# Kernel tuning notes

Hardware: AMD Instinct MI355X
Metric: run time of the kernel (lower is better)

## Reference

```python
import jax, jax.numpy as jnp
import numpy as np

EMBED = 1024
D_FF = 4 * EMBED
N_EXPERTS = 8
TOP_K = 2
B, S = 2, 1024


def setup_inputs() -> dict:
    key = jax.random.key(0)
    ks = jax.random.split(key, 10)
    sc_d = 1.0 / np.sqrt(EMBED)
    sc_h = 1.0 / np.sqrt(D_FF)
    return {
        "inputs": jax.random.normal(ks[0], (B, S, EMBED), jnp.float32),
        # router MLP: Linear(D,4D) -> ReLU -> Linear(4D,E)
        "rw1": jax.random.normal(ks[1], (EMBED, D_FF), jnp.float32) * sc_d,
        "rb1": jnp.zeros((D_FF,), jnp.float32),
        "rw2": jax.random.normal(ks[2], (D_FF, N_EXPERTS), jnp.float32) * sc_h,
        "rb2": jnp.zeros((N_EXPERTS,), jnp.float32),
        # stacked expert weights: Linear(D,4D) -> ReLU -> Linear(4D,D)
        "W1": jax.random.normal(ks[3], (N_EXPERTS, EMBED, D_FF), jnp.float32) * sc_d,
        "b1": jnp.zeros((N_EXPERTS, D_FF), jnp.float32),
        "W2": jax.random.normal(ks[4], (N_EXPERTS, D_FF, EMBED), jnp.float32) * sc_h,
        "b2": jnp.zeros((N_EXPERTS, EMBED), jnp.float32),
    }


def reference(inputs, rw1, rb1, rw2, rb2, W1, b1, W2, b2):
    Bb, Ss, D = inputs.shape
    T = Bb * Ss
    xf = inputs.reshape(T, D)  # [T, D]

    # Router: scores over experts, keep top-k, softmax over kept entries only.
    score = jax.nn.relu(xf @ rw1 + rb1) @ rw2 + rb2          # [T, E]
    _, topi = jax.lax.top_k(score, TOP_K)                    # [T, K]
    mask = jnp.zeros(score.shape, bool).at[jnp.arange(T)[:, None], topi].set(True)
    gate = jax.nn.softmax(jnp.where(mask, score, -jnp.inf), axis=-1)  # [T, E]

    # Dense per-expert MLP weighted by gate; gate==0 for non-top-k experts,
    # matching the original masked gather/scatter exactly.
    out = jnp.zeros_like(xf)
    for e in range(N_EXPERTS):
        h = jax.nn.relu(xf @ W1[e] + b1[e])                  # [T, 4D]
        y = h @ W2[e] + b2[e]                                # [T, D]
        out = out + gate[:, e:e + 1] * y
    return out.reshape(Bb, Ss, D)
```

## Files before the change

### kernel.cpp

```cpp
#include <hip/hip_runtime.h>
#include <stdint.h>

typedef unsigned short ushort_t;
typedef __attribute__((ext_vector_type(8))) short short8;
typedef __attribute__((ext_vector_type(4))) float f32x4;

#define EMBED   1024
#define DFF     4096
#define NEXP    8
#define TOKENS  2048
#define SLOTS   4096
#define TMAX    40

__device__ __forceinline__ ushort_t f2bf(float f) {
  unsigned u = __float_as_uint(f);
  u += 0x7FFFu + ((u >> 16) & 1u);
  return (ushort_t)(u >> 16);
}
__device__ __forceinline__ float bf2f(ushort_t b) {
  return __uint_as_float(((unsigned)b) << 16);
}

__device__ __forceinline__ void gl2lds16(const void* g, void* l) {
  typedef const __attribute__((address_space(1))) unsigned char* gp_t;
  typedef __attribute__((address_space(3))) unsigned char* lp_t;
  __builtin_amdgcn_global_load_lds((gp_t)(uintptr_t)g, (lp_t)(uintptr_t)l, 16, 0, 0);
}

__global__ void zero_small(int* counts, int* cursors) {
  int i = threadIdx.x;
  if (i < NEXP) { counts[i] = 0; cursors[i] = 0; }
}

__global__ void split_xhl(const float* __restrict__ x, ushort_t* __restrict__ Xs) {
  int t = blockIdx.x;
  int d = threadIdx.x * 4;
  float4 v = *(const float4*)(x + (size_t)t * EMBED + d);
  ushort4 hi, lo;
  hi.x = f2bf(v.x); lo.x = f2bf(v.x - bf2f(hi.x));
  hi.y = f2bf(v.y); lo.y = f2bf(v.y - bf2f(hi.y));
  hi.z = f2bf(v.z); lo.z = f2bf(v.z - bf2f(hi.z));
  hi.w = f2bf(v.w); lo.w = f2bf(v.w - bf2f(hi.w));
  ushort_t* row = Xs + (size_t)t * 2048;
  *(ushort4*)(row + d)        = hi;
  *(ushort4*)(row + 1024 + d) = lo;
}

__global__ void transp_conv(const float* __restrict__ src, ushort_t* __restrict__ dst,
                            int src_ld, int dst_ld, long src_estride, long dst_estride,
                            int dst_koff, int lo)
{
  __shared__ float t[64][65];
  const float* s = src + (size_t)blockIdx.z * src_estride;
  ushort_t* d = dst + (size_t)blockIdx.z * dst_estride;
  int n0 = blockIdx.x * 64, k0 = blockIdx.y * 64;
  int tid = threadIdx.x;
  int kk = tid >> 4, nn = (tid & 15) * 4;
  #pragma unroll
  for (int it = 0; it < 4; it++) {
    float4 v = *(const float4*)(s + (size_t)(k0 + kk + it * 16) * src_ld + n0 + nn);
    t[kk + it * 16][nn]     = v.x;
    t[kk + it * 16][nn + 1] = v.y;
    t[kk + it * 16][nn + 2] = v.z;
    t[kk + it * 16][nn + 3] = v.w;
  }
  __syncthreads();
  int nn2 = tid >> 3, kk2 = (tid & 7) * 8;
  #pragma unroll
  for (int it = 0; it < 2; it++) {
    int n = nn2 + it * 32;
    union { ushort_t u[8]; uint4 v; } pk;
    #pragma unroll
    for (int j = 0; j < 8; j++) {
      float xv = t[kk2 + j][n];
      ushort_t hv = f2bf(xv);
      pk.u[j] = lo ? f2bf(xv - bf2f(hv)) : hv;
    }
    *(uint4*)(d + (size_t)(n0 + n) * dst_ld + dst_koff + k0 + kk2) = pk.v;
  }
}

template<int APATH, int OUTMODE, bool RELU, bool EXPERT, int SPLITK, int NX>
__global__ __launch_bounds__(256, (OUTMODE == 4 ? 3 : 4))
void gemm_kernel(const ushort_t* __restrict__ A, const ushort_t* __restrict__ B,
                 const float* __restrict__ bias, void* __restrict__ Cout,
                 const float* __restrict__ slot_gate, const int* __restrict__ slot_token,
                 const int* __restrict__ off, const int* __restrict__ tile_e,
                 const int* __restrict__ tile_y, int e0, int e1,
                 int M, int N, int K)
{
  __shared__ ushort_t As[2][128 * 32];
  __shared__ ushort_t Bs[2][128 * 32];

  int e = 0, kc = 0, row0, col0, m_base, m_cnt;
  if (EXPERT) {
    int bid  = blockIdx.x;
    int xi   = bid % NX;
    int rest = bid / NX;
    kc       = rest % SPLITK;
    int t    = rest / SPLITK;
    e = tile_e[t];
    if (e < e0 || e >= e1) return;
    row0   = tile_y[t] * 128;
    col0   = xi * 128;
    m_base = off[e];
    m_cnt  = off[e + 1] - m_base;
  } else {
    row0 = blockIdx.y * 128;
    col0 = blockIdx.x * 128;
    m_base = 0; m_cnt = M;
    if (row0 >= m_cnt) return;
  }
  const int Kc   = K / SPLITK;
  const int kbeg = kc * Kc;

  const int tid  = threadIdx.x;
  const int lane = tid & 63;
  const int wid  = tid >> 6;
  const int wm = wid & 1, wn = wid >> 1;

  const int srow  = lane >> 2;
  const int schk8 = ((lane & 3) ^ ((lane >> 3) & 3)) * 8;

  const ushort_t* gA[2];
  const ushort_t* gB[2];
  int aoff[2];
  const ushort_t* Bt = B + (EXPERT ? (size_t)(e - e0) * (size_t)N * K : 0);
  #pragma unroll
  for (int h = 0; h < 2; h++) {
    int r  = row0 + h * 64 + wid * 16 + srow;
    int rl = min(r, m_cnt - 1);
    size_t rowb;
    if (APATH == 2)      rowb = (size_t)slot_token[m_base + rl] * 2048;
    else if (APATH == 1) rowb = (size_t)rl * 2048;
    else                 rowb = (size_t)(m_base + rl) * (size_t)K;
    gA[h]   = A + rowb + (APATH == 0 ? kbeg : 0) + schk8;
    aoff[h] = (h * 64 + wid * 16) * 32;

    int n = col0 + h * 64 + wid * 16 + srow;
    gB[h] = Bt + (size_t)n * K + kbeg + schk8;
  }

  auto stage = [&](int pb, int k0) {
    const int k0a = (APATH == 1 && k0 >= 2048) ? k0 - 2048 : k0;
    #pragma unroll
    for (int h = 0; h < 2; h++) {
      gl2lds16(gA[h] + k0a, &As[pb][aoff[h]]);
      gl2lds16(gB[h] + k0,  &Bs[pb][aoff[h]]);
    }
  };

  f32x4 acc[4][4];
  #pragma unroll
  for (int i = 0; i < 4; i++)
    #pragma unroll
    for (int j = 0; j < 4; j++)
      acc[i][j] = (f32x4){0.f, 0.f, 0.f, 0.f};

  const int q  = lane >> 4;
  const int rr = lane & 15;
  const int sw8 = (q ^ ((rr >> 1) & 3)) * 8;
  const int abase = (wm * 64 + rr) * 32 + sw8;
  const int bbase = (wn * 64 + rr) * 32 + sw8;

  const int nkt = Kc >> 5;

  stage(0, 0);
  __syncthreads();

  for (int kt = 0; kt < nkt; kt++) {
    const int cur = kt & 1, nxt = cur ^ 1;
    if (kt + 1 < nkt) stage(nxt, (kt + 1) << 5);

    short8 af[4], bfr[4];
    #pragma unroll
    for (int i = 0; i < 4; i++) {
      af[i]  = *(const short8*)(&As[cur][abase + i * 512]);
      bfr[i] = *(const short8*)(&Bs[cur][bbase + i * 512]);
    }
    #pragma unroll
    for (int mt = 0; mt < 4; mt++)
      #pragma unroll
      for (int nt = 0; nt < 4; nt++)
        acc[mt][nt] = __builtin_amdgcn_mfma_f32_16x16x32_bf16(af[mt], bfr[nt], acc[mt][nt], 0, 0, 0);

    __syncthreads();
  }

  const float* biasp = bias + (EXPERT ? (size_t)e * N : 0);
  float bv[4];
  #pragma unroll
  for (int nt = 0; nt < 4; nt++)
    bv[nt] = biasp[col0 + wn * 64 + nt * 16 + rr];
  const float bscale = (SPLITK == 1 || kc == 0) ? 1.f : 0.f;

  if constexpr (OUTMODE == 4) {
    const float* rw2p = slot_gate;
    float4 wa[4], wb[4];
    #pragma unroll
    for (int nt = 0; nt < 4; nt++) {
      int c = col0 + wn * 64 + nt * 16 + rr;
      wa[nt] = *(const float4*)(rw2p + (size_t)c * 8);
      wb[nt] = *(const float4*)(rw2p + (size_t)c * 8 + 4);
    }
    float* Ps = (float*)Cout;
    const int xi2 = (col0 >> 6) + wn;
    #pragma unroll
    for (int mt = 0; mt < 4; mt++) {
      #pragma unroll
      for (int i = 0; i < 4; i++) {
        float4 sA = {0.f, 0.f, 0.f, 0.f}, sB = {0.f, 0.f, 0.f, 0.f};
        #pragma unroll
        for (int nt = 0; nt < 4; nt++) {
          float v = acc[mt][nt][i] + bv[nt];
          if (RELU) v = fmaxf(v, 0.f);
          sA.x += v * wa[nt].x; sA.y += v * wa[nt].y;
          sA.z += v * wa[nt].z; sA.w += v * wa[nt].w;
          sB.x += v * wb[nt].x; sB.y += v * wb[nt].y;
          sB.z += v * wb[nt].z; sB.w += v * wb[nt].w;
        }
        #pragma unroll
        for (int o = 1; o <= 8; o <<= 1) {
          sA.x += __shfl_xor(sA.x, o); sA.y += __shfl_xor(sA.y, o);
          sA.z += __shfl_xor(sA.z, o); sA.w += __shfl_xor(sA.w, o);
          sB.x += __shfl_xor(sB.x, o); sB.y += __shfl_xor(sB.y, o);
          sB.z += __shfl_xor(sB.z, o); sB.w += __shfl_xor(sB.w, o);
        }
        if (rr == 0) {
          int row = row0 + wm * 64 + mt * 16 + q * 4 + i;
          float* p = Ps + ((size_t)row * 64 + xi2) * 8;
          *(float4*)p       = sA;
          *(float4*)(p + 4) = sB;
        }
      }
    }
  } else {
    #pragma unroll
    for (int mt = 0; mt < 4; mt++) {
      #pragma unroll
      for (int i = 0; i < 4; i++) {
        int r_loc = row0 + wm * 64 + mt * 16 + q * 4 + i;
        if (r_loc < m_cnt) {
          int slot = m_base + r_loc;
          float g = 1.f;
          if (OUTMODE == 3) g = slot_gate[slot];
          #pragma unroll
          for (int nt = 0; nt < 4; nt++) {
            float v = acc[mt][nt][i] + bscale * bv[nt];
            if (RELU) v = fmaxf(v, 0.f);
            int c = col0 + wn * 64 + nt * 16 + rr;
            if (OUTMODE == 0)      ((float*)Cout)[(size_t)slot * N + c]    = v;
            else if (OUTMODE == 1) ((ushort_t*)Cout)[(size_t)slot * N + c] = f2bf(v);
            else ((float*)Cout)[((size_t)kc * SLOTS + slot) * N + c] = g * v;
          }
        }
      }
    }
  }
}

__global__ void router_reduce(const float* __restrict__ Ps, const float* __restrict__ rb2,
                              int* __restrict__ topi, float* __restrict__ gates,
                              int* __restrict__ counts)
{
  int t = blockIdx.x * 4 + (threadIdx.x >> 6);
  if (t >= TOKENS) return;
  int lane = threadIdx.x & 63;
  const float* pt = Ps + (size_t)t * 512;
  float4 v0 = *(const float4*)(pt + lane * 8);
  float4 v1 = *(const float4*)(pt + lane * 8 + 4);
  #pragma unroll
  for (int o = 1; o <= 32; o <<= 1) {
    v0.x += __shfl_xor(v0.x, o); v0.y += __shfl_xor(v0.y, o);
    v0.z += __shfl_xor(v0.z, o); v0.w += __shfl_xor(v0.w, o);
    v1.x += __shfl_xor(v1.x, o); v1.y += __shfl_xor(v1.y, o);
    v1.z += __shfl_xor(v1.z, o); v1.w += __shfl_xor(v1.w, o);
  }
  if (lane == 0) {
    float s[8] = {v0.x + rb2[0], v0.y + rb2[1], v0.z + rb2[2], v0.w + rb2[3],
                  v1.x + rb2[4], v1.y + rb2[5], v1.z + rb2[6], v1.w + rb2[7]};
    int i0 = 0;
    #pragma unroll
    for (int e = 1; e < 8; e++) if (s[e] > s[i0]) i0 = e;
    int i1 = (i0 == 0) ? 1 : 0;
    #pragma unroll
    for (int e = 0; e < 8; e++) if (e != i0 && s[e] > s[i1]) i1 = e;
    float ex = __expf(s[i1] - s[i0]);
    float g0 = 1.f / (1.f + ex);
    float g1 = ex / (1.f + ex);
    topi[t * 2] = i0; topi[t * 2 + 1] = i1;
    gates[t * 2] = g0; gates[t * 2 + 1] = g1;
    atomicAdd(&counts[i0], 1);
    atomicAdd(&counts[i1], 1);
  }
}

__global__ void prefix_off(const int* __restrict__ counts, int* __restrict__ off,
                           int* __restrict__ tile_e, int* __restrict__ tile_y)
{
  if (threadIdx.x == 0) {
    int a = 0, t = 0;
    for (int e = 0; e < NEXP; e++) {
      off[e] = a;
      int c = counts[e]; a += c;
      int ty = (c + 127) >> 7;
      for (int y = 0; y < ty; y++) { tile_e[t] = e; tile_y[t] = y; t++; }
    }
    off[NEXP] = a;
    for (; t < TMAX; t++) { tile_e[t] = -1; tile_y[t] = 0; }
  }
}

__global__ void assign_slots(const int* __restrict__ topi, const float* __restrict__ gates,
                             const int* __restrict__ off, int* __restrict__ cursors,
                             int* __restrict__ slot_token, float* __restrict__ slot_gate,
                             int* __restrict__ tok_slot)
{
  int t = blockIdx.x * blockDim.x + threadIdx.x;
  if (t >= TOKENS) return;
  #pragma unroll
  for (int k = 0; k < 2; k++) {
    int e = topi[t * 2 + k];
    int p = atomicAdd(&cursors[e], 1);
    int s = off[e] + p;
    slot_token[s] = t;
    slot_gate[s]  = gates[t * 2 + k];
    tok_slot[t * 2 + k] = s;
  }
}

template<int NC>
__global__ void combine_out(const float* __restrict__ Ys, const int* __restrict__ tok_slot,
                            float* __restrict__ out)
{
  int t = blockIdx.x;
  int d = threadIdx.x * 4;
  int s0 = tok_slot[t * 2], s1 = tok_slot[t * 2 + 1];
  float4 o = {0.f, 0.f, 0.f, 0.f};
  #pragma unroll
  for (int k = 0; k < NC; k++) {
    float4 a = *(const float4*)(Ys + ((size_t)k * SLOTS + s0) * EMBED + d);
    float4 b = *(const float4*)(Ys + ((size_t)k * SLOTS + s1) * EMBED + d);
    o.x += a.x + b.x;
    o.y += a.y + b.y;
    o.z += a.z + b.z;
    o.w += a.w + b.w;
  }
  *(float4*)(out + (size_t)t * EMBED + d) = o;
}

extern "C" void kernel_launch(void* const* d_in, const int* in_sizes, int n_in,
                              void* d_out, int out_size, void* d_ws, size_t ws_size,
                              hipStream_t stream)
{
  const float* x   = (const float*)d_in[0];
  const float* rw1 = (const float*)d_in[1];
  const float* rb1 = (const float*)d_in[2];
  const float* rw2 = (const float*)d_in[3];
  const float* rb2 = (const float*)d_in[4];
  const float* W1  = (const float*)d_in[5];
  const float* b1  = (const float*)d_in[6];
  const float* W2  = (const float*)d_in[7];
  const float* b2  = (const float*)d_in[8];
  float* out = (float*)d_out;
  char* ws = (char*)d_ws;

  const long W1ES = (long)EMBED * DFF;
  const long W2ES = (long)DFF * EMBED;
  const size_t SZ_R = (size_t)4096 * 4096 * 2;

  const bool FULL = ws_size >= ((size_t)300 << 20);

  if (FULL) {
    char* p = ws;
    ushort_t* W1T  = (ushort_t*)p;  p += (size_t)NEXP * DFF * EMBED * 2;
    ushort_t* W2T  = (ushort_t*)p;  p += (size_t)NEXP * EMBED * DFF * 2;
    ushort_t* RW1t = (ushort_t*)p;  p += (size_t)4096 * 3072 * 2;
    ushort_t* Hs   = (ushort_t*)p;  p += (size_t)SLOTS * DFF * 2;
    ushort_t* Xhl  = (ushort_t*)p;  p += (size_t)TOKENS * 2048 * 2;
    float*    Ys   = (float*)p;     p += (size_t)4 * SLOTS * EMBED * 4;
    float*    Ps   = (float*)p;     p += (size_t)TOKENS * 512 * 4;
    int*   topi       = (int*)p;    p += TOKENS * 2 * 4;
    float* gates      = (float*)p;  p += TOKENS * 2 * 4;
    int*   tok_slot   = (int*)p;    p += TOKENS * 2 * 4;
    int*   slot_token = (int*)p;    p += SLOTS * 4;
    float* slot_gate  = (float*)p;  p += SLOTS * 4;
    int*   counts     = (int*)p;    p += 256;
    int*   cursors    = (int*)p;    p += 256;
    int*   off        = (int*)p;    p += 256;
    int*   tile_e     = (int*)p;    p += 256;
    int*   tile_y     = (int*)p;    p += 256;

    zero_small<<<1, 64, 0, stream>>>(counts, cursors);
    split_xhl<<<TOKENS, 256, 0, stream>>>(x, Xhl);

    transp_conv<<<dim3(64, 16, 1), 256, 0, stream>>>(rw1, RW1t, DFF, 3072, 0, 0, 0,    0);
    transp_conv<<<dim3(64, 16, 1), 256, 0, stream>>>(rw1, RW1t, DFF, 3072, 0, 0, 1024, 0);
    transp_conv<<<dim3(64, 16, 1), 256, 0, stream>>>(rw1, RW1t, DFF, 3072, 0, 0, 2048, 1);

    gemm_kernel<1, 4, true, false, 1, 32>
        <<<dim3(32, 16, 1), 256, 0, stream>>>(Xhl, RW1t, rb1, Ps, rw2, nullptr,
                                              nullptr, nullptr, nullptr, 0, NEXP,
                                              TOKENS, DFF, 3072);
    router_reduce<<<512, 256, 0, stream>>>(Ps, rb2, topi, gates, counts);
    prefix_off  <<<1, 64, 0, stream>>>(counts, off, tile_e, tile_y);
    assign_slots<<<8, 256, 0, stream>>>(topi, gates, off, cursors, slot_token, slot_gate, tok_slot);

    transp_conv<<<dim3(64, 16, 8), 256, 0, stream>>>(W1, W1T, DFF, EMBED, W1ES, W1ES, 0, 0);
    gemm_kernel<2, 1, true, true, 1, 32>
        <<<dim3(32 * TMAX, 1, 1), 256, 0, stream>>>(Xhl, W1T, b1, Hs,
            nullptr, slot_token, off, tile_e, tile_y, 0, NEXP, 0, DFF, EMBED);

    transp_conv<<<dim3(16, 64, 8), 256, 0, stream>>>(W2, W2T, EMBED, DFF, W2ES, W2ES, 0, 0);
    gemm_kernel<0, 3, false, true, 4, 8>
        <<<dim3(8 * 4 * TMAX, 1, 1), 256, 0, stream>>>(Hs, W2T, b2, Ys,
            slot_gate, nullptr, off, tile_e, tile_y, 0, NEXP, 0, EMBED, DFF);

    combine_out<4><<<TOKENS, 256, 0, stream>>>(Ys, tok_slot, out);
  } else {
    ushort_t* RW1t = (ushort_t*)ws;
    ushort_t* WT   = (ushort_t*)ws;
    ushort_t* Hs   = (ushort_t*)(ws + SZ_R);
    ushort_t* Xhl  = (ushort_t*)(ws + 2 * SZ_R);
    float*    Ys   = (float*)(ws + 2 * SZ_R);
    char* p = ws + 3 * SZ_R;
    float* Ps         = (float*)p;  p += (size_t)TOKENS * 512 * 4;
    int*   topi       = (int*)p;    p += TOKENS * 2 * 4;
    float* gates      = (float*)p;  p += TOKENS * 2 * 4;
    int*   tok_slot   = (int*)p;    p += TOKENS * 2 * 4;
    int*   slot_token = (int*)p;    p += SLOTS * 4;
    float* slot_gate  = (float*)p;  p += SLOTS * 4;
    int*   counts     = (int*)p;    p += 256;
    int*   cursors    = (int*)p;    p += 256;
    int*   off        = (int*)p;    p += 256;
    int*   tile_e     = (int*)p;    p += 256;
    int*   tile_y     = (int*)p;    p += 256;

    zero_small<<<1, 64, 0, stream>>>(counts, cursors);
    split_xhl<<<TOKENS, 256, 0, stream>>>(x, Xhl);

    transp_conv<<<dim3(64, 16, 1), 256, 0, stream>>>(rw1, RW1t, DFF, 3072, 0, 0, 0,    0);
    transp_conv<<<dim3(64, 16, 1), 256, 0, stream>>>(rw1, RW1t, DFF, 3072, 0, 0, 1024, 0);
    transp_conv<<<dim3(64, 16, 1), 256, 0, stream>>>(rw1, RW1t, DFF, 3072, 0, 0, 2048, 1);

    gemm_kernel<1, 4, true, false, 1, 32>
        <<<dim3(32, 16, 1), 256, 0, stream>>>(Xhl, RW1t, rb1, Ps, rw2, nullptr,
                                              nullptr, nullptr, nullptr, 0, NEXP,
                                              TOKENS, DFF, 3072);
    router_reduce<<<512, 256, 0, stream>>>(Ps, rb2, topi, gates, counts);
    prefix_off  <<<1, 64, 0, stream>>>(counts, off, tile_e, tile_y);
    assign_slots<<<8, 256, 0, stream>>>(topi, gates, off, cursors, slot_token, slot_gate, tok_slot);

    for (int half = 0; half < 2; half++) {
      int e0 = half * 4;
      transp_conv<<<dim3(64, 16, 4), 256, 0, stream>>>(W1 + (size_t)e0 * W1ES, WT,
          DFF, EMBED, W1ES, W1ES, 0, 0);
      gemm_kernel<2, 1, true, true, 1, 32>
          <<<dim3(32 * TMAX, 1, 1), 256, 0, stream>>>(Xhl, WT, b1, Hs,
              nullptr, slot_token, off, tile_e, tile_y, e0, e0 + 4, 0, DFF, EMBED);
    }
    for (int half = 0; half < 2; half++) {
      int e0 = half * 4;
      transp_conv<<<dim3(16, 64, 4), 256, 0, stream>>>(W2 + (size_t)e0 * W2ES, WT,
          EMBED, DFF, W2ES, W2ES, 0, 0);
      gemm_kernel<0, 3, false, true, 2, 8>
          <<<dim3(8 * 2 * TMAX, 1, 1), 256, 0, stream>>>(Hs, WT, b2, Ys,
              slot_gate, nullptr, off, tile_e, tile_y, e0, e0 + 4, 0, EMBED, DFF);
    }

    combine_out<2><<<TOKENS, 256, 0, stream>>>(Ys, tok_slot, out);
  }
}
```

Baseline: 621.0 us.

## Triple-buffer GEMM LDS pipeline and remap expert blocks for XCD locality

Moves the GEMM main loop from double to triple buffering, with explicit vmcnt waits and a single barrier per k-step, so global-to-LDS loads run two stages ahead of the MFMA work. It also remaps the expert GEMM block index so that all N/split-K blocks of one token tile land on the same XCD, aiming for better L2 reuse of the A rows. Launch bounds drop to 3 blocks per CU to fit the larger LDS footprint, which may lower occupancy. The grid sizes are rounded up to multiples of 8 tile groups to match the new mapping.

```diff
diff --git a/kernel.cpp b/kernel.cpp
--- a/kernel.cpp
+++ b/kernel.cpp
@@ -11,6 +11,7 @@
 #define TOKENS  2048
 #define SLOTS   4096
 #define TMAX    40
+#define TG      ((TMAX + 7) / 8)
 
 __device__ __forceinline__ ushort_t f2bf(float f) {
   unsigned u = __float_as_uint(f);
@@ -81,7 +82,7 @@
 }
 
 template<int APATH, int OUTMODE, bool RELU, bool EXPERT, int SPLITK, int NX>
-__global__ __launch_bounds__(256, (OUTMODE == 4 ? 3 : 4))
+__global__ __launch_bounds__(256, 3)
 void gemm_kernel(const ushort_t* __restrict__ A, const ushort_t* __restrict__ B,
                  const float* __restrict__ bias, void* __restrict__ Cout,
                  const float* __restrict__ slot_gate, const int* __restrict__ slot_token,
@@ -89,16 +90,19 @@
                  const int* __restrict__ tile_y, int e0, int e1,
                  int M, int N, int K)
 {
-  __shared__ ushort_t As[2][128 * 32];
-  __shared__ ushort_t Bs[2][128 * 32];
+  __shared__ ushort_t As[3][128 * 32];
+  __shared__ ushort_t Bs[3][128 * 32];
 
   int e = 0, kc = 0, row0, col0, m_base, m_cnt;
   if (EXPERT) {
-    int bid  = blockIdx.x;
-    int xi   = bid % NX;
-    int rest = bid / NX;
-    kc       = rest % SPLITK;
-    int t    = rest / SPLITK;
+    constexpr int INNER = NX * SPLITK;
+    int bid = blockIdx.x;
+    int xcd = bid & 7;
+    int j   = bid >> 3;
+    int t   = xcd + 8 * (j / INNER);
+    int i   = j % INNER;
+    int xi  = i % NX;
+    kc      = i / NX;
     e = tile_e[t];
     if (e < e0 || e >= e1) return;
     row0   = tile_y[t] * 128;
@@ -141,7 +145,8 @@
     gB[h] = Bt + (size_t)n * K + kbeg + schk8;
   }
 
-  auto stage = [&](int pb, int k0) {
+  auto stage = [&](int pb, int kt) {
+    const int k0 = kt << 5;
     const int k0a = (APATH == 1 && k0 >= 2048) ? k0 - 2048 : k0;
     #pragma unroll
     for (int h = 0; h < 2; h++) {
@@ -166,25 +171,29 @@
   const int nkt = Kc >> 5;
 
   stage(0, 0);
-  __syncthreads();
+  if (nkt > 1) stage(1, 1);
 
   for (int kt = 0; kt < nkt; kt++) {
-    const int cur = kt & 1, nxt = cur ^ 1;
-    if (kt + 1 < nkt) stage(nxt, (kt + 1) << 5);
-
+    if (kt + 1 < nkt) asm volatile("s_waitcnt vmcnt(4)" ::: "memory");
+    else              asm volatile("s_waitcnt vmcnt(0)" ::: "memory");
+    __builtin_amdgcn_s_barrier();
+    __builtin_amdgcn_sched_barrier(0);
+    if (kt + 2 < nkt) stage((kt + 2) % 3, kt + 2);
+
+    const int cur = kt % 3;
     short8 af[4], bfr[4];
     #pragma unroll
     for (int i = 0; i < 4; i++) {
       af[i]  = *(const short8*)(&As[cur][abase + i * 512]);
       bfr[i] = *(const short8*)(&Bs[cur][bbase + i * 512]);
     }
+    asm volatile("s_waitcnt lgkmcnt(0)" ::: "memory");
+    __builtin_amdgcn_sched_barrier(0);
     #pragma unroll
     for (int mt = 0; mt < 4; mt++)
       #pragma unroll
       for (int nt = 0; nt < 4; nt++)
         acc[mt][nt] = __builtin_amdgcn_mfma_f32_16x16x32_bf16(af[mt], bfr[nt], acc[mt][nt], 0, 0, 0);
-
-    __syncthreads();
   }
 
   const float* biasp = bias + (EXPERT ? (size_t)e * N : 0);
@@ -408,12 +417,12 @@
 
     transp_conv<<<dim3(64, 16, 8), 256, 0, stream>>>(W1, W1T, DFF, EMBED, W1ES, W1ES, 0, 0);
     gemm_kernel<2, 1, true, true, 1, 32>
-        <<<dim3(32 * TMAX, 1, 1), 256, 0, stream>>>(Xhl, W1T, b1, Hs,
+        <<<dim3(8 * TG * 32, 1, 1), 256, 0, stream>>>(Xhl, W1T, b1, Hs,
             nullptr, slot_token, off, tile_e, tile_y, 0, NEXP, 0, DFF, EMBED);
 
     transp_conv<<<dim3(16, 64, 8), 256, 0, stream>>>(W2, W2T, EMBED, DFF, W2ES, W2ES, 0, 0);
     gemm_kernel<0, 3, false, true, 4, 8>
-        <<<dim3(8 * 4 * TMAX, 1, 1), 256, 0, stream>>>(Hs, W2T, b2, Ys,
+        <<<dim3(8 * TG * 32, 1, 1), 256, 0, stream>>>(Hs, W2T, b2, Ys,
             slot_gate, nullptr, off, tile_e, tile_y, 0, NEXP, 0, EMBED, DFF);
 
     combine_out<4><<<TOKENS, 256, 0, stream>>>(Ys, tok_slot, out);
@@ -456,7 +465,7 @@
       transp_conv<<<dim3(64, 16, 4), 256, 0, stream>>>(W1 + (size_t)e0 * W1ES, WT,
           DFF, EMBED, W1ES, W1ES, 0, 0);
       gemm_kernel<2, 1, true, true, 1, 32>
-          <<<dim3(32 * TMAX, 1, 1), 256, 0, stream>>>(Xhl, WT, b1, Hs,
+          <<<dim3(8 * TG * 32, 1, 1), 256, 0, stream>>>(Xhl, WT, b1, Hs,
               nullptr, slot_token, off, tile_e, tile_y, e0, e0 + 4, 0, DFF, EMBED);
     }
     for (int half = 0; half < 2; half++) {
@@ -464,7 +473,7 @@
       transp_conv<<<dim3(16, 64, 4), 256, 0, stream>>>(W2 + (size_t)e0 * W2ES, WT,
           EMBED, DFF, W2ES, W2ES, 0, 0);
       gemm_kernel<0, 3, false, true, 2, 8>
-          <<<dim3(8 * 2 * TMAX, 1, 1), 256, 0, stream>>>(Hs, WT, b2, Ys,
+          <<<dim3(8 * TG * 16, 1, 1), 256, 0, stream>>>(Hs, WT, b2, Ys,
               slot_gate, nullptr, off, tile_e, tile_y, e0, e0 + 4, 0, EMBED, DFF);
     }
 
```

New measurement: 617.3 us. No clear change (-0.6%).
